# Performance work log

Hardware: AMD Instinct MI355X
Metric: run time of the kernel (lower is better)

## Reference

```python
import jax, jax.numpy as jnp
import numpy as np

N, NS, CIN, COUT, S = 65536, 16, 64, 64, 8
MID = COUT  # mid_planes = out_planes // 1
EPS = 1e-5


def _bn(t, g, b):
    # BatchNorm1d in training mode: normalize per channel over (points, neighbors)
    m = jnp.mean(t, axis=(0, 1), keepdims=True)
    v = jnp.var(t, axis=(0, 1), keepdims=True)
    return (t - m) * jax.lax.rsqrt(v + EPS) * g + b


def setup_inputs() -> dict:
    key = jax.random.key(0)
    ks = jax.random.split(key, 16)

    def w(k, shape, fan_in):
        return (jax.random.normal(k, shape, jnp.float32) / np.sqrt(fan_in)).astype(jnp.float32)

    return {
        "p": jax.random.uniform(ks[0], (N, 3), jnp.float32),
        "x": jax.random.normal(ks[1], (N, CIN), jnp.float32),
        "idx": jax.random.randint(ks[2], (N, NS), 0, N, jnp.int32),
        # q/k/v linears
        "Wq": w(ks[3], (CIN, MID), CIN), "bq": jnp.zeros((MID,), jnp.float32),
        "Wk": w(ks[4], (CIN, MID), CIN), "bk": jnp.zeros((MID,), jnp.float32),
        "Wv": w(ks[5], (CIN, COUT), CIN), "bv": jnp.zeros((COUT,), jnp.float32),
        # linear_p: Linear(3,3) -> BN(3) -> ReLU -> Linear(3,out)
        "Wp1": w(ks[6], (3, 3), 3), "bp1": jnp.zeros((3,), jnp.float32),
        "gp": jnp.ones((3,), jnp.float32), "bp_bn": jnp.zeros((3,), jnp.float32),
        "Wp2": w(ks[7], (3, COUT), 3), "bp2": jnp.zeros((COUT,), jnp.float32),
        # linear_w: BN(mid)->ReLU->Linear(mid,mid//s)->BN->ReLU->Linear(mid//s,mid//s)
        "gw1": jnp.ones((MID,), jnp.float32), "bw1_bn": jnp.zeros((MID,), jnp.float32),
        "Ww1": w(ks[8], (MID, MID // S), MID), "bw1": jnp.zeros((MID // S,), jnp.float32),
        "gw2": jnp.ones((MID // S,), jnp.float32), "bw2_bn": jnp.zeros((MID // S,), jnp.float32),
        "Ww2": w(ks[9], (MID // S, MID // S), MID // S), "bw2": jnp.zeros((MID // S,), jnp.float32),
    }


def reference(p, x, idx, Wq, bq, Wk, bk, Wv, bv, Wp1, bp1, gp, bp_bn, Wp2, bp2,
              gw1, bw1_bn, Ww1, bw1, gw2, bw2_bn, Ww2, bw2):
    # per-point projections
    xq = x @ Wq + bq                       # [N, MID]
    xk = x @ Wk + bk                       # [N, MID]
    xv = x @ Wv + bv                       # [N, COUT]
    # queryandgroup: gather neighbor features + relative xyz
    rel_p = p[idx] - p[:, None, :]         # [N, NS, 3]
    xk_g = xk[idx]                         # [N, NS, MID]
    xv_g = xv[idx]                         # [N, NS, COUT]
    # linear_p MLP on relative positions
    pr = rel_p @ Wp1 + bp1
    pr = jax.nn.relu(_bn(pr, gp, bp_bn))
    pr = pr @ Wp2 + bp2                    # [N, NS, COUT]
    # subtractive attention logits (out//mid == 1, so p_r sum is identity)
    w = xk_g - xq[:, None, :] + pr         # [N, NS, MID]
    # linear_w MLP
    w = jax.nn.relu(_bn(w, gw1, bw1_bn))
    w = w @ Ww1 + bw1                      # [N, NS, MID//S]
    w = jax.nn.relu(_bn(w, gw2, bw2_bn))
    w = w @ Ww2 + bw2                      # [N, NS, COUT//S]
    w = jax.nn.softmax(w, axis=1)          # softmax over neighbors
    # grouped weighted aggregation with shared attention planes
    n, ns, c = xv_g.shape
    out = ((xv_g + pr).reshape(n, ns, S, c // S) * w[:, :, None, :]).sum(1)
    return out.reshape(n, c)
```

## Files before the change

### kernel.cpp

```cpp
#include <hip/hip_runtime.h>

typedef unsigned short u16;
typedef __attribute__((ext_vector_type(8))) short bf16x8;
typedef __attribute__((ext_vector_type(2))) float f32x2;
typedef __attribute__((ext_vector_type(4))) float f32x4;

#define NPTS 65536
#define MTOT 1048576
#define M2TOT 131072
#define EPSb 1e-5f

#define XQ_OFF  0u
#define T_OFF   4194304u
#define ST_OFF  15728640u
#define XK_US   31457792u
#define XV_US   35652096u

__device__ __forceinline__ float bf2f(u16 h) {
    return __uint_as_float(((unsigned)h) << 16);
}
__device__ __forceinline__ u16 f2bf(float f) {
    unsigned u = __float_as_uint(f);
    u += 0x7fffu + ((u >> 16) & 1u);
    return (u16)(u >> 16);
}
__device__ __forceinline__ unsigned cvt_pk_bf16(float lo, float hi) {
    unsigned r;
    asm("v_cvt_pk_bf16_f32 %0, %1, %2" : "=v"(r) : "v"(lo), "v"(hi));
    return r;
}
__device__ __forceinline__ bf16x8 pack_bf8(const float4 lo, const float4 hi) {
    union { bf16x8 v; unsigned u[4]; } r;
    r.u[0] = cvt_pk_bf16(lo.x, lo.y);
    r.u[1] = cvt_pk_bf16(lo.z, lo.w);
    r.u[2] = cvt_pk_bf16(hi.x, hi.y);
    r.u[3] = cvt_pk_bf16(hi.z, hi.w);
    return r.v;
}

struct BN2C {
    f32x2 A2[4], D[4], W0[4], W1[4], W2[4];
};
__device__ __forceinline__ void bn2c_build(
    BN2C& c, const int kbase, const float* __restrict__ ws,
    const float* __restrict__ gw1, const float* __restrict__ bw1_bn,
    const float* __restrict__ bp2, const float* __restrict__ Wp2)
{
    const float invM2 = 1.0f / (float)M2TOT;
#pragma unroll
    for (int j = 0; j < 4; ++j) {
        float a2[2], d[2], w0[2], w1[2], w2[2];
#pragma unroll
        for (int h = 0; h < 2; ++h) {
            const int k = kbase + 2 * j + h;
            const float mean = ws[ST_OFF + 6 + k] * invM2;
            const float var  = ws[ST_OFF + 70 + k] * invM2 - mean * mean;
            const float A2 = gw1[k] * rsqrtf(var + EPSb);
            const float B2 = bw1_bn[k] - mean * A2;
            a2[h] = A2; d[h] = fmaf(A2, bp2[k], B2);
            w0[h] = A2 * Wp2[k]; w1[h] = A2 * Wp2[64 + k]; w2[h] = A2 * Wp2[128 + k];
        }
        c.A2[j] = f32x2{a2[0], a2[1]}; c.D[j] = f32x2{d[0], d[1]};
        c.W0[j] = f32x2{w0[0], w0[1]}; c.W1[j] = f32x2{w1[0], w1[1]};
        c.W2[j] = f32x2{w2[0], w2[1]};
    }
}
__device__ __forceinline__ bf16x8 build_frag(
    const BN2C& c, const f32x2 t0v, const f32x2 t1v, const f32x2 t2v,
    const uint4 g, const float4 xlo, const float4 xhi)
{
    union { bf16x8 v; unsigned u[4]; } r;
    const unsigned gu[4] = { g.x, g.y, g.z, g.w };
    const f32x2 xp[4] = { {xlo.x, xlo.y}, {xlo.z, xlo.w}, {xhi.x, xhi.y}, {xhi.z, xhi.w} };
#pragma unroll
    for (int j = 0; j < 4; ++j) {
        f32x2 gf;
        gf.x = __uint_as_float(gu[j] << 16);
        gf.y = __uint_as_float(gu[j] & 0xffff0000u);
        f32x2 v = c.D[j] - c.A2[j] * xp[j];
        v = v + t0v * c.W0[j];
        v = v + t1v * c.W1[j];
        v = v + t2v * c.W2[j];
        v = v + c.A2[j] * gf;
        r.u[j] = cvt_pk_bf16(fmaxf(v.x, 0.0f), fmaxf(v.y, 0.0f));
    }
    return r.v;
}

__device__ __forceinline__ void load_b_frags(
    const float* __restrict__ Ww1, const int col16, const int quad,
    bf16x8& b0, bf16x8& b1)
{
    b0 = bf16x8{0,0,0,0,0,0,0,0};
    b1 = bf16x8{0,0,0,0,0,0,0,0};
    if (col16 < 8) {
#pragma unroll
        for (int j = 0; j < 8; ++j) {
            const int k0 = quad * 8 + j;
            b0[j] = (short)f2bf(Ww1[k0 * 8 + col16]);
            b1[j] = (short)f2bf(Ww1[(k0 + 32) * 8 + col16]);
        }
    }
}

__global__ __launch_bounds__(256) void k1_proj_bn1(
    const float* __restrict__ p, const float* __restrict__ x, const int* __restrict__ idx,
    const float* __restrict__ Wq, const float* __restrict__ Wk, const float* __restrict__ Wv,
    const float* __restrict__ bq, const float* __restrict__ bk, const float* __restrict__ bv,
    const float* __restrict__ Wp1, const float* __restrict__ bp1,
    float* __restrict__ ws)
{
    u16* wsu = (u16*)ws;
    __shared__ u16 wtab[12288];
    __shared__ float sred[6];
    const int tid   = threadIdx.x;
    const int lane  = tid & 63;
    const int wid   = tid >> 6;
    const int col16 = lane & 15;
    const int quad  = lane >> 4;
    if (tid < 6) sred[tid] = 0.0f;

#pragma unroll
    for (int k = 0; k < 48; ++k) {
        const int e = tid + k * 256;
        const float* W = (e < 4096) ? Wq : ((e < 8192) ? Wk : Wv);
        const int rem = e & 4095;
        const int n = rem >> 6, c = rem & 63;
        wtab[e] = f2bf(W[c * 64 + n]);
    }
    __syncthreads();

    bf16x8 bf[3][4][2];
#pragma unroll
    for (int M = 0; M < 3; ++M)
#pragma unroll
        for (int t = 0; t < 4; ++t)
#pragma unroll
            for (int h = 0; h < 2; ++h)
                bf[M][t][h] = *(const bf16x8*)&wtab[
                    (unsigned)(M * 4096 + (t * 16 + col16) * 64 + h * 32 + quad * 8)];

    float bq_t[4], bk_t[4], bv_t[4];
#pragma unroll
    for (int t = 0; t < 4; ++t) {
        bq_t[t] = bq[t * 16 + col16];
        bk_t[t] = bk[t * 16 + col16];
        bv_t[t] = bv[t * 16 + col16];
    }

    float* xq   = ws + XQ_OFF;
    u16*  xkb   = wsu + XK_US;
    u16*  xvb   = wsu + XV_US;

    const int gw = blockIdx.x * 4 + wid;
#pragma unroll
    for (int g = 0; g < 2; ++g) {
        const int n0 = (gw * 2 + g) * 16;
        const float* xrow = x + (unsigned)(n0 + col16) * 64u;
        const float4 fa0 = *(const float4*)&xrow[quad * 8];
        const float4 fa1 = *(const float4*)&xrow[quad * 8 + 4];
        const float4 fb0 = *(const float4*)&xrow[32 + quad * 8];
        const float4 fb1 = *(const float4*)&xrow[32 + quad * 8 + 4];
        const bf16x8 a0 = pack_bf8(fa0, fa1);
        const bf16x8 a1 = pack_bf8(fb0, fb1);

#pragma unroll
        for (int t = 0; t < 4; ++t) {
            f32x4 aq = {0,0,0,0}, ak = {0,0,0,0}, av = {0,0,0,0};
            aq = __builtin_amdgcn_mfma_f32_16x16x32_bf16(a0, bf[0][t][0], aq, 0, 0, 0);
            aq = __builtin_amdgcn_mfma_f32_16x16x32_bf16(a1, bf[0][t][1], aq, 0, 0, 0);
            ak = __builtin_amdgcn_mfma_f32_16x16x32_bf16(a0, bf[1][t][0], ak, 0, 0, 0);
            ak = __builtin_amdgcn_mfma_f32_16x16x32_bf16(a1, bf[1][t][1], ak, 0, 0, 0);
            av = __builtin_amdgcn_mfma_f32_16x16x32_bf16(a0, bf[2][t][0], av, 0, 0, 0);
            av = __builtin_amdgcn_mfma_f32_16x16x32_bf16(a1, bf[2][t][1], av, 0, 0, 0);
#pragma unroll
            for (int r = 0; r < 4; ++r) {
                const unsigned row = (unsigned)(n0 + quad * 4 + r);
                const unsigned o   = row * 64u + (unsigned)(t * 16 + col16);
                xq[o]  = aq[r] + bq_t[t];
                xkb[o] = f2bf(ak[r] + bk_t[t]);
                xvb[o] = f2bf(av[r] + bv_t[t]);
            }
        }
    }

    const int base = blockIdx.x * 128;
    const float w00 = Wp1[0], w01 = Wp1[1], w02 = Wp1[2];
    const float w10 = Wp1[3], w11 = Wp1[4], w12 = Wp1[5];
    const float w20 = Wp1[6], w21 = Wp1[7], w22 = Wp1[8];
    const float c0 = bp1[0], c1 = bp1[1], c2 = bp1[2];
    float s0 = 0, s1 = 0, s2 = 0, q0 = 0, q1 = 0, q2 = 0;
#pragma unroll
    for (int m = 0; m < 8; ++m) {
        const int pl = tid + m * 256;
        const int n  = base + (pl >> 4);
        const unsigned gpair = (unsigned)(base * 16 + pl);
        const int nb = idx[gpair];
        const float r0 = p[nb * 3 + 0] - p[n * 3 + 0];
        const float r1 = p[nb * 3 + 1] - p[n * 3 + 1];
        const float r2 = p[nb * 3 + 2] - p[n * 3 + 2];
        const float t0 = c0 + r0 * w00 + r1 * w10 + r2 * w20;
        const float t1 = c1 + r0 * w01 + r1 * w11 + r2 * w21;
        const float t2 = c2 + r0 * w02 + r1 * w12 + r2 * w22;
        ws[T_OFF + gpair * 3u + 0u] = t0;
        ws[T_OFF + gpair * 3u + 1u] = t1;
        ws[T_OFF + gpair * 3u + 2u] = t2;
        s0 += t0; s1 += t1; s2 += t2;
        q0 += t0 * t0; q1 += t1 * t1; q2 += t2 * t2;
    }
    atomicAdd(&sred[0], s0); atomicAdd(&sred[1], s1); atomicAdd(&sred[2], s2);
    atomicAdd(&sred[3], q0); atomicAdd(&sred[4], q1); atomicAdd(&sred[5], q2);
    __syncthreads();
    if (tid < 6) atomicAdd(&ws[ST_OFF + tid], sred[tid]);
}

__global__ __launch_bounds__(256) void k1b_bn1apply(
    const float* __restrict__ gp, const float* __restrict__ bp_bn,
    float* __restrict__ ws)
{
    const float invM = 1.0f / (float)MTOT;
    float A1[3], B1[3];
#pragma unroll
    for (int a = 0; a < 3; ++a) {
        const float mean = ws[ST_OFF + a] * invM;
        const float var  = ws[ST_OFF + 3 + a] * invM - mean * mean;
        const float sc = gp[a] * rsqrtf(var + EPSb);
        A1[a] = sc; B1[a] = bp_bn[a] - mean * sc;
    }
    const unsigned t = blockIdx.x * 256u + threadIdx.x;
    float4* Tp = (float4*)(ws + T_OFF + t * 12u);
    float4 v0 = Tp[0], v1 = Tp[1], v2 = Tp[2];
    v0.x = fmaxf(fmaf(v0.x, A1[0], B1[0]), 0.0f);
    v0.y = fmaxf(fmaf(v0.y, A1[1], B1[1]), 0.0f);
    v0.z = fmaxf(fmaf(v0.z, A1[2], B1[2]), 0.0f);
    v0.w = fmaxf(fmaf(v0.w, A1[0], B1[0]), 0.0f);
    v1.x = fmaxf(fmaf(v1.x, A1[1], B1[1]), 0.0f);
    v1.y = fmaxf(fmaf(v1.y, A1[2], B1[2]), 0.0f);
    v1.z = fmaxf(fmaf(v1.z, A1[0], B1[0]), 0.0f);
    v1.w = fmaxf(fmaf(v1.w, A1[1], B1[1]), 0.0f);
    v2.x = fmaxf(fmaf(v2.x, A1[2], B1[2]), 0.0f);
    v2.y = fmaxf(fmaf(v2.y, A1[0], B1[0]), 0.0f);
    v2.z = fmaxf(fmaf(v2.z, A1[1], B1[1]), 0.0f);
    v2.w = fmaxf(fmaf(v2.w, A1[2], B1[2]), 0.0f);
    Tp[0] = v0; Tp[1] = v1; Tp[2] = v2;
}

__global__ __launch_bounds__(256) void k2_bn2(
    const int* __restrict__ idx,
    const float* __restrict__ Wp2, const float* __restrict__ bp2,
    float* __restrict__ ws)
{
    u16* wsu = (u16*)ws;
    __shared__ float ss[64], sq[64];
    const int tid = threadIdx.x;
    const int lane = tid & 63;
    const int gw = blockIdx.x * 4 + (tid >> 6);
    if (tid < 64) { ss[tid] = 0.0f; sq[tid] = 0.0f; }

    const float wp20 = Wp2[lane], wp21 = Wp2[64 + lane], wp22 = Wp2[128 + lane];
    const float bp2c = bp2[lane];
    const float* xq  = ws + XQ_OFF;
    const float* T   = ws + T_OFF;
    const u16*  xkb  = wsu + XK_US;

    float s = 0.0f, q = 0.0f;

    for (int nn = 0; nn < 4; ++nn) {
        const int nu = __builtin_amdgcn_readfirstlane((gw * 4 + nn) * 8);

        const int4* ir4 = (const int4*)(idx + (unsigned)nu * 16u);
        const int4 i0 = ir4[0], i1 = ir4[1], i2 = ir4[2], i3 = ir4[3];
        const int nbs[16] = { i0.x, i0.y, i0.z, i0.w, i1.x, i1.y, i1.z, i1.w,
                              i2.x, i2.y, i2.z, i2.w, i3.x, i3.y, i3.z, i3.w };
        u16 kr[16];
#pragma unroll
        for (int j = 0; j < 16; ++j) kr[j] = xkb[(unsigned)nbs[j] * 64u + lane];

        float tr[48];
        const float4* Tr4 = (const float4*)(T + (unsigned)nu * 48u);
#pragma unroll
        for (int c = 0; c < 12; ++c) {
            const float4 v = Tr4[c];
            tr[4 * c + 0] = v.x; tr[4 * c + 1] = v.y;
            tr[4 * c + 2] = v.z; tr[4 * c + 3] = v.w;
        }
        const float xqc  = xq[(unsigned)nu * 64u + lane];
        const float base = bp2c - xqc;

#pragma unroll
        for (int j = 0; j < 16; ++j) {
            const float prx = base + tr[3 * j + 0] * wp20
                                   + tr[3 * j + 1] * wp21
                                   + tr[3 * j + 2] * wp22;
            const float w0 = bf2f(kr[j]) + prx;
            s += w0; q = fmaf(w0, w0, q);
        }
    }
    __syncthreads();
    atomicAdd(&ss[lane], s); atomicAdd(&sq[lane], q);
    __syncthreads();
    if (tid < 64) {
        atomicAdd(&ws[ST_OFF + 6 + tid], ss[tid]);
        atomicAdd(&ws[ST_OFF + 70 + tid], sq[tid]);
    }
}

__global__ __launch_bounds__(256) void k2b_bn3(
    const int* __restrict__ idx,
    const float* __restrict__ Wp2, const float* __restrict__ bp2,
    const float* __restrict__ gw1, const float* __restrict__ bw1_bn,
    const float* __restrict__ Ww1, const float* __restrict__ bw1,
    float* __restrict__ ws)
{
    u16* wsu = (u16*)ws;
    __shared__ float s3r[8], q3r[8];
    const int tid   = threadIdx.x;
    const int lane  = tid & 63;
    const int wid   = tid >> 6;
    const int col16 = lane & 15;
    const int quad  = lane >> 4;
    if (tid < 8) { s3r[tid] = 0.0f; q3r[tid] = 0.0f; }
    __syncthreads();

    BN2C cA, cB;
    bn2c_build(cA, quad * 8,      ws, gw1, bw1_bn, bp2, Wp2);
    bn2c_build(cB, 32 + quad * 8, ws, gw1, bw1_bn, bp2, Wp2);

    bf16x8 b0, b1;
    load_b_frags(Ww1, col16, quad, b0, b1);
    const float bw1c = (col16 < 8) ? bw1[col16] : 0.0f;

    const float* xq  = ws + XQ_OFF;
    const float* T   = ws + T_OFF;
    const u16*  xkb  = wsu + XK_US;
    const int sg = (blockIdx.x * 4 + wid) * 8;
    float bs = 0.0f, bq2 = 0.0f;

    for (int it = 0; it < 8; ++it) {
        const int nu = __builtin_amdgcn_readfirstlane((sg + it) * 8);

        const int nbv = idx[(unsigned)nu * 16u + (unsigned)col16];
        const u16* grow = xkb + (unsigned)nbv * 64u;
        const uint4 gA = *(const uint4*)(grow + quad * 8);
        const uint4 gB = *(const uint4*)(grow + 32 + quad * 8);

        const float* Trow = T + (unsigned)nu * 48u + (unsigned)col16 * 3u;
        const f32x2 t0v = f32x2{Trow[0], Trow[0]};
        const f32x2 t1v = f32x2{Trow[1], Trow[1]};
        const f32x2 t2v = f32x2{Trow[2], Trow[2]};

        const float* xr = xq + (unsigned)nu * 64u;
        const float4 x0 = *(const float4*)(xr + quad * 8);
        const float4 x1 = *(const float4*)(xr + quad * 8 + 4);
        const float4 x2 = *(const float4*)(xr + 32 + quad * 8);
        const float4 x3 = *(const float4*)(xr + 32 + quad * 8 + 4);

        const bf16x8 a0 = build_frag(cA, t0v, t1v, t2v, gA, x0, x1);
        const bf16x8 a1 = build_frag(cB, t0v, t1v, t2v, gB, x2, x3);

        f32x4 acc = {0.0f, 0.0f, 0.0f, 0.0f};
        acc = __builtin_amdgcn_mfma_f32_16x16x32_bf16(a0, b0, acc, 0, 0, 0);
        acc = __builtin_amdgcn_mfma_f32_16x16x32_bf16(a1, b1, acc, 0, 0, 0);
        if (col16 < 8) {
#pragma unroll
            for (int r = 0; r < 4; ++r) {
                const float o = acc[r] + bw1c;
                bs += o;
                bq2 = fmaf(o, o, bq2);
            }
        }
    }
    if (col16 < 8) {
        atomicAdd(&s3r[col16], bs);
        atomicAdd(&q3r[col16], bq2);
    }
    __syncthreads();
    if (tid < 8) {
        atomicAdd(&ws[ST_OFF + 134 + tid], s3r[tid]);
        atomicAdd(&ws[ST_OFF + 142 + tid], q3r[tid]);
    }
}

__global__ __launch_bounds__(256) void k34_fused(
    const int* __restrict__ idx,
    const float* __restrict__ Wp2, const float* __restrict__ bp2,
    const float* __restrict__ gw1, const float* __restrict__ bw1_bn,
    const float* __restrict__ Ww1, const float* __restrict__ bw1,
    const float* __restrict__ gw2, const float* __restrict__ bw2_bn,
    const float* __restrict__ Ww2, const float* __restrict__ bw2,
    const float* __restrict__ ws, float* __restrict__ out)
{
    const u16* wsu = (const u16*)ws;
    __shared__ float sv3[4][16][8];
    __shared__ float se[4][16][8];
    const int tid   = threadIdx.x;
    const int lane  = tid & 63;
    const int wid   = tid >> 6;
    const int col16 = lane & 15;
    const int quad  = lane >> 4;
    const int tt    = lane & 7;
    const int j1    = lane >> 3;

    const float invM2 = 1.0f / (float)M2TOT;
    BN2C cA, cB;
    bn2c_build(cA, quad * 8,      ws, gw1, bw1_bn, bp2, Wp2);
    bn2c_build(cB, 32 + quad * 8, ws, gw1, bw1_bn, bp2, Wp2);

    bf16x8 b0, b1;
    load_b_frags(Ww1, col16, quad, b0, b1);
    const float bw1c = (col16 < 8) ? bw1[col16] : 0.0f;
    const int   c3    = col16 & 7;
    const float mean3 = ws[ST_OFF + 134 + c3] * invM2;
    const float var3  = ws[ST_OFF + 142 + c3] * invM2 - mean3 * mean3;
    const float A3c   = gw2[c3] * rsqrtf(var3 + EPSb);
    const float B3f   = fmaf(A3c, bw1c, bw2_bn[c3] - mean3 * A3c);
    float ww2c[8];
#pragma unroll
    for (int u = 0; u < 8; ++u) ww2c[u] = Ww2[u * 8 + tt];
    const float bw2c = bw2[tt];
    const float wp20 = Wp2[lane], wp21 = Wp2[64 + lane], wp22 = Wp2[128 + lane];
    const float bp2c = bp2[lane];

    const float* xq  = ws + XQ_OFF;
    const float* T   = ws + T_OFF;
    const u16*  xkb  = wsu + XK_US;
    const u16*  xvb  = wsu + XV_US;

    const int n0 = (blockIdx.x * 4 + wid) * 8;
    for (int it = 0; it < 8; ++it) {
        const int nu = __builtin_amdgcn_readfirstlane(n0 + it);

        const int4* ir4 = (const int4*)(idx + (unsigned)nu * 16u);
        const int4 i0 = ir4[0], i1 = ir4[1], i2 = ir4[2], i3 = ir4[3];
        const int nbs[16] = { i0.x, i0.y, i0.z, i0.w, i1.x, i1.y, i1.z, i1.w,
                              i2.x, i2.y, i2.z, i2.w, i3.x, i3.y, i3.z, i3.w };
        const int nbv = idx[(unsigned)nu * 16u + (unsigned)col16];
        const u16* grow = xkb + (unsigned)nbv * 64u;
        const uint4 gA = *(const uint4*)(grow + quad * 8);
        const uint4 gB = *(const uint4*)(grow + 32 + quad * 8);
        u16 xvr[16];
#pragma unroll
        for (int j = 0; j < 16; ++j) xvr[j] = xvb[(unsigned)nbs[j] * 64u + lane];

        const float* Trow = T + (unsigned)nu * 48u + (unsigned)col16 * 3u;
        const f32x2 t0v = f32x2{Trow[0], Trow[0]};
        const f32x2 t1v = f32x2{Trow[1], Trow[1]};
        const f32x2 t2v = f32x2{Trow[2], Trow[2]};
        float tr[48];
        const float4* Tr4 = (const float4*)(T + (unsigned)nu * 48u);
#pragma unroll
        for (int c = 0; c < 12; ++c) {
            const float4 v = Tr4[c];
            tr[4 * c + 0] = v.x; tr[4 * c + 1] = v.y;
            tr[4 * c + 2] = v.z; tr[4 * c + 3] = v.w;
        }
        const float* xr = xq + (unsigned)nu * 64u;
        const float4 x0 = *(const float4*)(xr + quad * 8);
        const float4 x1 = *(const float4*)(xr + quad * 8 + 4);
        const float4 x2 = *(const float4*)(xr + 32 + quad * 8);
        const float4 x3 = *(const float4*)(xr + 32 + quad * 8 + 4);

        const bf16x8 a0 = build_frag(cA, t0v, t1v, t2v, gA, x0, x1);
        const bf16x8 a1 = build_frag(cB, t0v, t1v, t2v, gB, x2, x3);

        f32x4 acc = {0.0f, 0.0f, 0.0f, 0.0f};
        acc = __builtin_amdgcn_mfma_f32_16x16x32_bf16(a0, b0, acc, 0, 0, 0);
        acc = __builtin_amdgcn_mfma_f32_16x16x32_bf16(a1, b1, acc, 0, 0, 0);

        if (col16 < 8) {
#pragma unroll
            for (int r = 0; r < 4; ++r)
                sv3[wid][quad * 4 + r][col16] = fmaxf(fmaf(A3c, acc[r], B3f), 0.0f);
        }
        float s0 = bw2c, s1 = bw2c;
#pragma unroll
        for (int u = 0; u < 8; ++u) {
            s0 = fmaf(sv3[wid][j1][u], ww2c[u], s0);
            s1 = fmaf(sv3[wid][j1 + 8][u], ww2c[u], s1);
        }
        float mx = fmaxf(s0, s1);
        mx = fmaxf(mx, __shfl_xor(mx, 8));
        mx = fmaxf(mx, __shfl_xor(mx, 16));
        mx = fmaxf(mx, __shfl_xor(mx, 32));
        const float e0 = __expf(s0 - mx);
        const float e1 = __expf(s1 - mx);
        float sm = e0 + e1;
        sm += __shfl_xor(sm, 8);
        sm += __shfl_xor(sm, 16);
        sm += __shfl_xor(sm, 32);
        const float rs = __builtin_amdgcn_rcpf(sm);
        se[wid][j1][tt]     = e0 * rs;
        se[wid][j1 + 8][tt] = e1 * rs;

        float xvacc = 0.0f, ta0 = 0.0f, ta1 = 0.0f, ta2 = 0.0f;
#pragma unroll
        for (int j = 0; j < 16; ++j) {
            const float ej = se[wid][j][tt];
            xvacc = fmaf(bf2f(xvr[j]), ej, xvacc);
            ta0 = fmaf(tr[3 * j + 0], ej, ta0);
            ta1 = fmaf(tr[3 * j + 1], ej, ta1);
            ta2 = fmaf(tr[3 * j + 2], ej, ta2);
        }
        out[(unsigned)nu * 64u + lane] =
            fmaf(ta0, wp20, fmaf(ta1, wp21, fmaf(ta2, wp22, xvacc + bp2c)));
    }
}

extern "C" void kernel_launch(void* const* d_in, const int* in_sizes, int n_in,
                              void* d_out, int out_size, void* d_ws, size_t ws_size,
                              hipStream_t stream)
{
    const float* p      = (const float*)d_in[0];
    const float* x      = (const float*)d_in[1];
    const int*   idx    = (const int*)d_in[2];
    const float* Wq     = (const float*)d_in[3];
    const float* bq     = (const float*)d_in[4];
    const float* Wk     = (const float*)d_in[5];
    const float* bk     = (const float*)d_in[6];
    const float* Wv     = (const float*)d_in[7];
    const float* bv     = (const float*)d_in[8];
    const float* Wp1    = (const float*)d_in[9];
    const float* bp1    = (const float*)d_in[10];
    const float* gp     = (const float*)d_in[11];
    const float* bp_bn  = (const float*)d_in[12];
    const float* Wp2    = (const float*)d_in[13];
    const float* bp2    = (const float*)d_in[14];
    const float* gw1    = (const float*)d_in[15];
    const float* bw1_bn = (const float*)d_in[16];
    const float* Ww1    = (const float*)d_in[17];
    const float* bw1    = (const float*)d_in[18];
    const float* gw2    = (const float*)d_in[19];
    const float* bw2_bn = (const float*)d_in[20];
    const float* Ww2    = (const float*)d_in[21];
    const float* bw2    = (const float*)d_in[22];
    float* ws  = (float*)d_ws;
    float* out = (float*)d_out;
    (void)in_sizes; (void)n_in; (void)out_size; (void)ws_size;

    hipMemsetAsync((char*)d_ws + (size_t)ST_OFF * 4, 0, 150 * sizeof(float), stream);

    k1_proj_bn1<<<512, 256, 0, stream>>>(p, x, idx, Wq, Wk, Wv,
                                         bq, bk, bv, Wp1, bp1, ws);
    k1b_bn1apply<<<1024, 256, 0, stream>>>(gp, bp_bn, ws);
    k2_bn2<<<512, 256, 0, stream>>>(idx, Wp2, bp2, ws);
    k2b_bn3<<<256, 256, 0, stream>>>(idx, Wp2, bp2, gw1, bw1_bn, Ww1, bw1, ws);
    k34_fused<<<2048, 256, 0, stream>>>(idx, Wp2, bp2, gw1, bw1_bn, Ww1, bw1,
                                        gw2, bw2_bn, Ww2, bw2, ws, out);
}
```

Baseline: 271.3 us.

## Split BN1 stats pass from projection, fuse BN1 apply, precompute bf16 weight tables

A new lightweight first kernel computes only the BN1 moments over relative positions and writes bf16-transposed Wq/Wk/Wv and Ww1 tables to workspace. The projection kernel then recomputes the Wp1 transform and applies BN1+ReLU directly when writing T, which removes the separate read-modify-write apply pass and the extra round trip of T. Later kernels load the precomputed Ww1 bf16 fragments instead of converting per block. The final kernel now handles 16 points per wave with half the blocks. The cost is recomputing the gather of p and the 3x3 transform twice.

```diff
diff --git a/kernel.cpp b/kernel.cpp
--- a/kernel.cpp
+++ b/kernel.cpp
@@ -15,6 +15,8 @@
 #define ST_OFF  15728640u
 #define XK_US   31457792u
 #define XV_US   35652096u
+#define WTQ_US  14680064u
+#define WT1_US  14692352u
 
 __device__ __forceinline__ float bf2f(u16 h) {
     return __uint_as_float(((unsigned)h) << 16);
@@ -87,101 +89,29 @@
     return r.v;
 }
 
-__device__ __forceinline__ void load_b_frags(
-    const float* __restrict__ Ww1, const int col16, const int quad,
-    bf16x8& b0, bf16x8& b1)
-{
-    b0 = bf16x8{0,0,0,0,0,0,0,0};
-    b1 = bf16x8{0,0,0,0,0,0,0,0};
-    if (col16 < 8) {
-#pragma unroll
-        for (int j = 0; j < 8; ++j) {
-            const int k0 = quad * 8 + j;
-            b0[j] = (short)f2bf(Ww1[k0 * 8 + col16]);
-            b1[j] = (short)f2bf(Ww1[(k0 + 32) * 8 + col16]);
-        }
-    }
-}
-
-__global__ __launch_bounds__(256) void k1_proj_bn1(
-    const float* __restrict__ p, const float* __restrict__ x, const int* __restrict__ idx,
-    const float* __restrict__ Wq, const float* __restrict__ Wk, const float* __restrict__ Wv,
-    const float* __restrict__ bq, const float* __restrict__ bk, const float* __restrict__ bv,
+__global__ __launch_bounds__(256) void k0_mom_tab(
+    const float* __restrict__ p, const int* __restrict__ idx,
+    const float* __restrict__ Wq, const float* __restrict__ Wk,
+    const float* __restrict__ Wv, const float* __restrict__ Ww1,
     const float* __restrict__ Wp1, const float* __restrict__ bp1,
     float* __restrict__ ws)
 {
     u16* wsu = (u16*)ws;
-    __shared__ u16 wtab[12288];
     __shared__ float sred[6];
-    const int tid   = threadIdx.x;
-    const int lane  = tid & 63;
-    const int wid   = tid >> 6;
-    const int col16 = lane & 15;
-    const int quad  = lane >> 4;
+    const int tid = threadIdx.x;
+    const int gid = blockIdx.x * 256 + tid;
     if (tid < 6) sred[tid] = 0.0f;
-
-#pragma unroll
-    for (int k = 0; k < 48; ++k) {
-        const int e = tid + k * 256;
-        const float* W = (e < 4096) ? Wq : ((e < 8192) ? Wk : Wv);
-        const int rem = e & 4095;
+    __syncthreads();
+
+    if (gid < 12288) {
+        const float* W = (gid < 4096) ? Wq : ((gid < 8192) ? Wk : Wv);
+        const int rem = gid & 4095;
         const int n = rem >> 6, c = rem & 63;
-        wtab[e] = f2bf(W[c * 64 + n]);
-    }
-    __syncthreads();
-
-    bf16x8 bf[3][4][2];
-#pragma unroll
-    for (int M = 0; M < 3; ++M)
-#pragma unroll
-        for (int t = 0; t < 4; ++t)
-#pragma unroll
-            for (int h = 0; h < 2; ++h)
-                bf[M][t][h] = *(const bf16x8*)&wtab[
-                    (unsigned)(M * 4096 + (t * 16 + col16) * 64 + h * 32 + quad * 8)];
-
-    float bq_t[4], bk_t[4], bv_t[4];
-#pragma unroll
-    for (int t = 0; t < 4; ++t) {
-        bq_t[t] = bq[t * 16 + col16];
-        bk_t[t] = bk[t * 16 + col16];
-        bv_t[t] = bv[t * 16 + col16];
-    }
-
-    float* xq   = ws + XQ_OFF;
-    u16*  xkb   = wsu + XK_US;
-    u16*  xvb   = wsu + XV_US;
-
-    const int gw = blockIdx.x * 4 + wid;
-#pragma unroll
-    for (int g = 0; g < 2; ++g) {
-        const int n0 = (gw * 2 + g) * 16;
-        const float* xrow = x + (unsigned)(n0 + col16) * 64u;
-        const float4 fa0 = *(const float4*)&xrow[quad * 8];
-        const float4 fa1 = *(const float4*)&xrow[quad * 8 + 4];
-        const float4 fb0 = *(const float4*)&xrow[32 + quad * 8];
-        const float4 fb1 = *(const float4*)&xrow[32 + quad * 8 + 4];
-        const bf16x8 a0 = pack_bf8(fa0, fa1);
-        const bf16x8 a1 = pack_bf8(fb0, fb1);
-
-#pragma unroll
-        for (int t = 0; t < 4; ++t) {
-            f32x4 aq = {0,0,0,0}, ak = {0,0,0,0}, av = {0,0,0,0};
-            aq = __builtin_amdgcn_mfma_f32_16x16x32_bf16(a0, bf[0][t][0], aq, 0, 0, 0);
-            aq = __builtin_amdgcn_mfma_f32_16x16x32_bf16(a1, bf[0][t][1], aq, 0, 0, 0);
-            ak = __builtin_amdgcn_mfma_f32_16x16x32_bf16(a0, bf[1][t][0], ak, 0, 0, 0);
-            ak = __builtin_amdgcn_mfma_f32_16x16x32_bf16(a1, bf[1][t][1], ak, 0, 0, 0);
-            av = __builtin_amdgcn_mfma_f32_16x16x32_bf16(a0, bf[2][t][0], av, 0, 0, 0);
-            av = __builtin_amdgcn_mfma_f32_16x16x32_bf16(a1, bf[2][t][1], av, 0, 0, 0);
-#pragma unroll
-            for (int r = 0; r < 4; ++r) {
-                const unsigned row = (unsigned)(n0 + quad * 4 + r);
-                const unsigned o   = row * 64u + (unsigned)(t * 16 + col16);
-                xq[o]  = aq[r] + bq_t[t];
-                xkb[o] = f2bf(ak[r] + bk_t[t]);
-                xvb[o] = f2bf(av[r] + bv_t[t]);
-            }
-        }
+        wsu[WTQ_US + (unsigned)gid] = f2bf(W[c * 64 + n]);
+    } else if (gid < 12800) {
+        const int rem = gid - 12288;
+        const int c = rem >> 6, r = rem & 63;
+        wsu[WT1_US + (unsigned)rem] = f2bf(Ww1[r * 8 + c]);
     }
 
     const int base = blockIdx.x * 128;
@@ -202,9 +132,6 @@
         const float t0 = c0 + r0 * w00 + r1 * w10 + r2 * w20;
         const float t1 = c1 + r0 * w01 + r1 * w11 + r2 * w21;
         const float t2 = c2 + r0 * w02 + r1 * w12 + r2 * w22;
-        ws[T_OFF + gpair * 3u + 0u] = t0;
-        ws[T_OFF + gpair * 3u + 1u] = t1;
-        ws[T_OFF + gpair * 3u + 2u] = t2;
         s0 += t0; s1 += t1; s2 += t2;
         q0 += t0 * t0; q1 += t1 * t1; q2 += t2 * t2;
     }
@@ -214,10 +141,20 @@
     if (tid < 6) atomicAdd(&ws[ST_OFF + tid], sred[tid]);
 }
 
-__global__ __launch_bounds__(256) void k1b_bn1apply(
+__global__ __launch_bounds__(256) void k1_proj(
+    const float* __restrict__ p, const float* __restrict__ x, const int* __restrict__ idx,
+    const float* __restrict__ bq, const float* __restrict__ bk, const float* __restrict__ bv,
+    const float* __restrict__ Wp1, const float* __restrict__ bp1,
     const float* __restrict__ gp, const float* __restrict__ bp_bn,
     float* __restrict__ ws)
 {
+    u16* wsu = (u16*)ws;
+    const int tid   = threadIdx.x;
+    const int lane  = tid & 63;
+    const int wid   = tid >> 6;
+    const int col16 = lane & 15;
+    const int quad  = lane >> 4;
+
     const float invM = 1.0f / (float)MTOT;
     float A1[3], B1[3];
 #pragma unroll
@@ -227,22 +164,82 @@
         const float sc = gp[a] * rsqrtf(var + EPSb);
         A1[a] = sc; B1[a] = bp_bn[a] - mean * sc;
     }
-    const unsigned t = blockIdx.x * 256u + threadIdx.x;
-    float4* Tp = (float4*)(ws + T_OFF + t * 12u);
-    float4 v0 = Tp[0], v1 = Tp[1], v2 = Tp[2];
-    v0.x = fmaxf(fmaf(v0.x, A1[0], B1[0]), 0.0f);
-    v0.y = fmaxf(fmaf(v0.y, A1[1], B1[1]), 0.0f);
-    v0.z = fmaxf(fmaf(v0.z, A1[2], B1[2]), 0.0f);
-    v0.w = fmaxf(fmaf(v0.w, A1[0], B1[0]), 0.0f);
-    v1.x = fmaxf(fmaf(v1.x, A1[1], B1[1]), 0.0f);
-    v1.y = fmaxf(fmaf(v1.y, A1[2], B1[2]), 0.0f);
-    v1.z = fmaxf(fmaf(v1.z, A1[0], B1[0]), 0.0f);
-    v1.w = fmaxf(fmaf(v1.w, A1[1], B1[1]), 0.0f);
-    v2.x = fmaxf(fmaf(v2.x, A1[2], B1[2]), 0.0f);
-    v2.y = fmaxf(fmaf(v2.y, A1[0], B1[0]), 0.0f);
-    v2.z = fmaxf(fmaf(v2.z, A1[1], B1[1]), 0.0f);
-    v2.w = fmaxf(fmaf(v2.w, A1[2], B1[2]), 0.0f);
-    Tp[0] = v0; Tp[1] = v1; Tp[2] = v2;
+
+    bf16x8 bf[3][4][2];
+#pragma unroll
+    for (int M = 0; M < 3; ++M)
+#pragma unroll
+        for (int t = 0; t < 4; ++t)
+#pragma unroll
+            for (int h = 0; h < 2; ++h)
+                bf[M][t][h] = *(const bf16x8*)&wsu[WTQ_US +
+                    (unsigned)(M * 4096 + (t * 16 + col16) * 64 + h * 32 + quad * 8)];
+
+    float bq_t[4], bk_t[4], bv_t[4];
+#pragma unroll
+    for (int t = 0; t < 4; ++t) {
+        bq_t[t] = bq[t * 16 + col16];
+        bk_t[t] = bk[t * 16 + col16];
+        bv_t[t] = bv[t * 16 + col16];
+    }
+
+    float* xq   = ws + XQ_OFF;
+    u16*  xkb   = wsu + XK_US;
+    u16*  xvb   = wsu + XV_US;
+
+    const int gw = blockIdx.x * 4 + wid;
+#pragma unroll
+    for (int g = 0; g < 2; ++g) {
+        const int n0 = (gw * 2 + g) * 16;
+        const float* xrow = x + (unsigned)(n0 + col16) * 64u;
+        const float4 fa0 = *(const float4*)&xrow[quad * 8];
+        const float4 fa1 = *(const float4*)&xrow[quad * 8 + 4];
+        const float4 fb0 = *(const float4*)&xrow[32 + quad * 8];
+        const float4 fb1 = *(const float4*)&xrow[32 + quad * 8 + 4];
+        const bf16x8 a0 = pack_bf8(fa0, fa1);
+        const bf16x8 a1 = pack_bf8(fb0, fb1);
+
+#pragma unroll
+        for (int t = 0; t < 4; ++t) {
+            f32x4 aq = {0,0,0,0}, ak = {0,0,0,0}, av = {0,0,0,0};
+            aq = __builtin_amdgcn_mfma_f32_16x16x32_bf16(a0, bf[0][t][0], aq, 0, 0, 0);
+            aq = __builtin_amdgcn_mfma_f32_16x16x32_bf16(a1, bf[0][t][1], aq, 0, 0, 0);
+            ak = __builtin_amdgcn_mfma_f32_16x16x32_bf16(a0, bf[1][t][0], ak, 0, 0, 0);
+            ak = __builtin_amdgcn_mfma_f32_16x16x32_bf16(a1, bf[1][t][1], ak, 0, 0, 0);
+            av = __builtin_amdgcn_mfma_f32_16x16x32_bf16(a0, bf[2][t][0], av, 0, 0, 0);
+            av = __builtin_amdgcn_mfma_f32_16x16x32_bf16(a1, bf[2][t][1], av, 0, 0, 0);
+#pragma unroll
+            for (int r = 0; r < 4; ++r) {
+                const unsigned row = (unsigned)(n0 + quad * 4 + r);
+                const unsigned o   = row * 64u + (unsigned)(t * 16 + col16);
+                xq[o]  = aq[r] + bq_t[t];
+                xkb[o] = f2bf(ak[r] + bk_t[t]);
+                xvb[o] = f2bf(av[r] + bv_t[t]);
+            }
+        }
+    }
+
+    const int base = blockIdx.x * 128;
+    const float w00 = Wp1[0], w01 = Wp1[1], w02 = Wp1[2];
+    const float w10 = Wp1[3], w11 = Wp1[4], w12 = Wp1[5];
+    const float w20 = Wp1[6], w21 = Wp1[7], w22 = Wp1[8];
+    const float c0 = bp1[0], c1 = bp1[1], c2 = bp1[2];
+#pragma unroll
+    for (int m = 0; m < 8; ++m) {
+        const int pl = tid + m * 256;
+        const int n  = base + (pl >> 4);
+        const unsigned gpair = (unsigned)(base * 16 + pl);
+        const int nb = idx[gpair];
+        const float r0 = p[nb * 3 + 0] - p[n * 3 + 0];
+        const float r1 = p[nb * 3 + 1] - p[n * 3 + 1];
+        const float r2 = p[nb * 3 + 2] - p[n * 3 + 2];
+        const float t0 = c0 + r0 * w00 + r1 * w10 + r2 * w20;
+        const float t1 = c1 + r0 * w01 + r1 * w11 + r2 * w21;
+        const float t2 = c2 + r0 * w02 + r1 * w12 + r2 * w22;
+        ws[T_OFF + gpair * 3u + 0u] = fmaxf(fmaf(t0, A1[0], B1[0]), 0.0f);
+        ws[T_OFF + gpair * 3u + 1u] = fmaxf(fmaf(t1, A1[1], B1[1]), 0.0f);
+        ws[T_OFF + gpair * 3u + 2u] = fmaxf(fmaf(t2, A1[2], B1[2]), 0.0f);
+    }
 }
 
 __global__ __launch_bounds__(256) void k2_bn2(
@@ -309,7 +306,7 @@
     const int* __restrict__ idx,
     const float* __restrict__ Wp2, const float* __restrict__ bp2,
     const float* __restrict__ gw1, const float* __restrict__ bw1_bn,
-    const float* __restrict__ Ww1, const float* __restrict__ bw1,
+    const float* __restrict__ bw1,
     float* __restrict__ ws)
 {
     u16* wsu = (u16*)ws;
@@ -326,8 +323,11 @@
     bn2c_build(cA, quad * 8,      ws, gw1, bw1_bn, bp2, Wp2);
     bn2c_build(cB, 32 + quad * 8, ws, gw1, bw1_bn, bp2, Wp2);
 
-    bf16x8 b0, b1;
-    load_b_frags(Ww1, col16, quad, b0, b1);
+    bf16x8 b0 = {0,0,0,0,0,0,0,0}, b1 = {0,0,0,0,0,0,0,0};
+    if (col16 < 8) {
+        b0 = *(const bf16x8*)&wsu[WT1_US + (unsigned)(col16 * 64 + quad * 8)];
+        b1 = *(const bf16x8*)&wsu[WT1_US + (unsigned)(col16 * 64 + 32 + quad * 8)];
+    }
     const float bw1c = (col16 < 8) ? bw1[col16] : 0.0f;
 
     const float* xq  = ws + XQ_OFF;
@@ -385,7 +385,7 @@
     const int* __restrict__ idx,
     const float* __restrict__ Wp2, const float* __restrict__ bp2,
     const float* __restrict__ gw1, const float* __restrict__ bw1_bn,
-    const float* __restrict__ Ww1, const float* __restrict__ bw1,
+    const float* __restrict__ bw1,
     const float* __restrict__ gw2, const float* __restrict__ bw2_bn,
     const float* __restrict__ Ww2, const float* __restrict__ bw2,
     const float* __restrict__ ws, float* __restrict__ out)
@@ -406,8 +406,11 @@
     bn2c_build(cA, quad * 8,      ws, gw1, bw1_bn, bp2, Wp2);
     bn2c_build(cB, 32 + quad * 8, ws, gw1, bw1_bn, bp2, Wp2);
 
-    bf16x8 b0, b1;
-    load_b_frags(Ww1, col16, quad, b0, b1);
+    bf16x8 b0 = {0,0,0,0,0,0,0,0}, b1 = {0,0,0,0,0,0,0,0};
+    if (col16 < 8) {
+        b0 = *(const bf16x8*)&wsu[WT1_US + (unsigned)(col16 * 64 + quad * 8)];
+        b1 = *(const bf16x8*)&wsu[WT1_US + (unsigned)(col16 * 64 + 32 + quad * 8)];
+    }
     const float bw1c = (col16 < 8) ? bw1[col16] : 0.0f;
     const int   c3    = col16 & 7;
     const float mean3 = ws[ST_OFF + 134 + c3] * invM2;
@@ -426,8 +429,8 @@
     const u16*  xkb  = wsu + XK_US;
     const u16*  xvb  = wsu + XV_US;
 
-    const int n0 = (blockIdx.x * 4 + wid) * 8;
-    for (int it = 0; it < 8; ++it) {
+    const int n0 = (blockIdx.x * 4 + wid) * 16;
+    for (int it = 0; it < 16; ++it) {
         const int nu = __builtin_amdgcn_readfirstlane(n0 + it);
 
         const int4* ir4 = (const int4*)(idx + (unsigned)nu * 16u);
@@ -539,11 +542,10 @@
 
     hipMemsetAsync((char*)d_ws + (size_t)ST_OFF * 4, 0, 150 * sizeof(float), stream);
 
-    k1_proj_bn1<<<512, 256, 0, stream>>>(p, x, idx, Wq, Wk, Wv,
-                                         bq, bk, bv, Wp1, bp1, ws);
-    k1b_bn1apply<<<1024, 256, 0, stream>>>(gp, bp_bn, ws);
+    k0_mom_tab<<<512, 256, 0, stream>>>(p, idx, Wq, Wk, Wv, Ww1, Wp1, bp1, ws);
+    k1_proj<<<512, 256, 0, stream>>>(p, x, idx, bq, bk, bv, Wp1, bp1, gp, bp_bn, ws);
     k2_bn2<<<512, 256, 0, stream>>>(idx, Wp2, bp2, ws);
-    k2b_bn3<<<256, 256, 0, stream>>>(idx, Wp2, bp2, gw1, bw1_bn, Ww1, bw1, ws);
-    k34_fused<<<2048, 256, 0, stream>>>(idx, Wp2, bp2, gw1, bw1_bn, Ww1, bw1,
+    k2b_bn3<<<256, 256, 0, stream>>>(idx, Wp2, bp2, gw1, bw1_bn, bw1, ws);
+    k34_fused<<<1024, 256, 0, stream>>>(idx, Wp2, bp2, gw1, bw1_bn, bw1,
                                         gw2, bw2_bn, Ww2, bw2, ws, out);
 }
```

After: 253.0 us, median of 2. 1.07x faster.
